# Kernel optimization log

Hardware: AMD Instinct MI355X
Metric: run time of the kernel (lower is better)

## Reference

```python
import jax, jax.numpy as jnp
import numpy as np


def _boxsum(x):
    # x: [C, H, W] -> depthwise 3x3 all-ones sum conv, SAME padding (ChannelWiseSum(C, 3))
    C = x.shape[0]
    k = jnp.ones((C, 1, 3, 3), x.dtype)
    y = jax.lax.conv_general_dilated(
        x[None], k, window_strides=(1, 1), padding='SAME',
        dimension_numbers=('NCHW', 'OIHW', 'NCHW'), feature_group_count=C)
    return y[0]


def setup_inputs() -> dict:
    key = jax.random.key(0)
    k1, k2 = jax.random.split(key)
    H = W = 4096
    rgb = jax.random.uniform(k1, (3, H, W), dtype=jnp.float32)
    # alpha in [0,1] with ~half the pixels exactly 0 so the border diffusion is exercised
    a = jax.random.uniform(k2, (1, H, W), dtype=jnp.float32) * 2.0 - 1.0
    alpha = jnp.maximum(a, 0.0)
    return {"rgb": rgb, "alpha": alpha, "offset": 16}


def reference(rgb, alpha, offset):
    # rgb: [3,H,W], alpha: [1,H,W], offset: python int (number of diffusion steps)
    mask = (alpha > 0.0).astype(rgb.dtype)           # [1,H,W]
    rgb = rgb * mask

    def step(carry, _):
        rgb, mask = carry
        mask_nega = jnp.abs(mask - 1.0)              # [1,H,W], broadcasts over channels
        mask_weight = _boxsum(mask)                  # [1,H,W]
        border = _boxsum(rgb) / (mask_weight + 1e-7) # [3,H,W]
        border = border * mask_nega
        rgb = rgb * mask + border
        mask = (mask_weight > 0.0).astype(rgb.dtype)
        return (rgb, mask), None

    (rgb, _), _ = jax.lax.scan(step, (rgb, mask), None, length=offset)
    return jnp.clip(rgb, 0.0, 1.0)
```

## Files before the change

kernel.cpp:

```cpp
#include <hip/hip_runtime.h>

constexpr int W = 4096;
constexpr int H = 4096;
constexpr int HW = W * H;

constexpr int BX = 32, BY = 8;
constexpr int TILE_W = BX * 4;
constexpr int GRID_X = W / TILE_W;
constexpr int GRID_Y = H / BY;

typedef unsigned char u8;
typedef unsigned int u32;

__device__ __forceinline__ float clamp01(float v) { return fminf(fmaxf(v, 0.f), 1.f); }
__device__ __forceinline__ float4 ld4(const float* p) { return *reinterpret_cast<const float4*>(p); }
__device__ __forceinline__ void st4(float* p, float4 v) { *reinterpret_cast<float4*>(p) = v; }
__device__ __forceinline__ float4 z4() { return make_float4(0.f, 0.f, 0.f, 0.f); }
__device__ __forceinline__ float rcp_f(float x) { return __builtin_amdgcn_rcpf(x); }

__device__ __attribute__((noinline)) u32 far_distance(
    const float* __restrict__ alpha, int x, int y)
{
    for (int dy = -2; dy <= 2; ++dy) {
        int yy = y + dy;
        if (yy < 0 || yy >= H) continue;
        if (dy == -2 || dy == 2) {
            for (int dx = -2; dx <= 2; ++dx) {
                int xx = x + dx;
                if (xx < 0 || xx >= W) continue;
                if (alpha[yy * W + xx] > 0.f) return 2;
            }
        } else {
            if (x - 2 >= 0 && alpha[yy * W + x - 2] > 0.f) return 2;
            if (x + 2 < W && alpha[yy * W + x + 2] > 0.f) return 2;
        }
    }
    for (int r = 3; r <= 16; ++r) {
        bool f = false;
        for (int dx = -r; dx <= r && !f; ++dx) {
            int gx = x + dx;
            if (gx < 0 || gx >= W) continue;
            int gy = y - r;
            if (gy >= 0 && alpha[gy * W + gx] > 0.f) f = true;
            gy = y + r;
            if (!f && gy < H && alpha[gy * W + gx] > 0.f) f = true;
        }
        for (int dy = -r + 1; dy <= r - 1 && !f; ++dy) {
            int gy = y + dy;
            if (gy < 0 || gy >= H) continue;
            int gx = x - r;
            if (gx >= 0 && alpha[gy * W + gx] > 0.f) f = true;
            gx = x + r;
            if (!f && gx < W && alpha[gy * W + gx] > 0.f) f = true;
        }
        if (f) return r;
    }
    return 255;
}

__device__ __forceinline__ float4 plane_vsum(const float* __restrict__ base, int p0,
                                             bool up, bool dn,
                                             float4 mU, float4 mC, float4 mD,
                                             float4* center)
{
    float4 u = up ? ld4(base + p0 - W) : z4();
    float4 c = ld4(base + p0);
    float4 d = dn ? ld4(base + p0 + W) : z4();
    *center = c;
    float4 r;
    r.x = u.x * mU.x + c.x * mC.x + d.x * mD.x;
    r.y = u.y * mU.y + c.y * mC.y + d.y * mD.y;
    r.z = u.z * mU.z + c.z * mC.z + d.z * mD.z;
    r.w = u.w * mU.w + c.w * mC.w + d.w * mD.w;
    return r;
}

__global__ __launch_bounds__(BX * BY) void pass1_kernel(
    const float* __restrict__ rgb, const float* __restrict__ alpha,
    float* __restrict__ out, u8* __restrict__ dmap,
    u32* __restrict__ cnt, int* __restrict__ list, u32 cap)
{
    __shared__ __align__(16) float vs[4][BY][132];

    const int tx = threadIdx.x, ty = threadIdx.y;
    const int x0 = blockIdx.x * TILE_W + tx * 4;
    const int y  = blockIdx.y * BY + ty;
    const int p0 = y * W + x0;

    const bool up = (y > 0), dn = (y < H - 1);

    float4 aU = up ? ld4(alpha + p0 - W) : z4();
    float4 aC = ld4(alpha + p0);
    float4 aD = dn ? ld4(alpha + p0 + W) : z4();

    float4 mU = make_float4(aU.x > 0.f, aU.y > 0.f, aU.z > 0.f, aU.w > 0.f);
    float4 mC = make_float4(aC.x > 0.f, aC.y > 0.f, aC.z > 0.f, aC.w > 0.f);
    float4 mD = make_float4(aD.x > 0.f, aD.y > 0.f, aD.z > 0.f, aD.w > 0.f);

    float4 vwt;
    vwt.x = mU.x + mC.x + mD.x;
    vwt.y = mU.y + mC.y + mD.y;
    vwt.z = mU.z + mC.z + mD.z;
    vwt.w = mU.w + mC.w + mD.w;

    const float* Gp = rgb + HW;
    const float* Bp = rgb + 2 * HW;

    float4 rC, gC, bC;
    float4 vr = plane_vsum(rgb, p0, up, dn, mU, mC, mD, &rC);
    float4 vg = plane_vsum(Gp,  p0, up, dn, mU, mC, mD, &gC);
    float4 vb = plane_vsum(Bp,  p0, up, dn, mU, mC, mD, &bC);

    st4(&vs[0][ty][tx * 4], vr);
    st4(&vs[1][ty][tx * 4], vg);
    st4(&vs[2][ty][tx * 4], vb);
    st4(&vs[3][ty][tx * 4], vwt);

    if (tx == 0 || tx == BX - 1) {
        int xh   = (tx == 0) ? x0 - 1 : x0 + 4;
        int slot = (tx == 0) ? 130 : 128;
        float sr = 0.f, sg = 0.f, sb = 0.f, sw = 0.f;
        if (xh >= 0 && xh < W) {
            #pragma unroll
            for (int dy = -1; dy <= 1; ++dy) {
                int yy = y + dy;
                if (yy < 0 || yy >= H) continue;
                int q = yy * W + xh;
                float m = (alpha[q] > 0.f) ? 1.f : 0.f;
                sw += m;
                sr += m * rgb[q];
                sg += m * Gp[q];
                sb += m * Bp[q];
            }
        }
        vs[0][ty][slot] = sr;
        vs[1][ty][slot] = sg;
        vs[2][ty][slot] = sb;
        vs[3][ty][slot] = sw;
    }
    __syncthreads();

    const int cL = (tx == 0) ? 130 : tx * 4 - 1;
    const int cR = (tx == BX - 1) ? 128 : tx * 4 + 4;

    float sr[4], sg[4], sb[4], sw[4];
    {
        float4 v = ld4(&vs[0][ty][tx * 4]);
        float l = vs[0][ty][cL], r = vs[0][ty][cR];
        sr[0] = l + v.x + v.y; sr[1] = v.x + v.y + v.z;
        sr[2] = v.y + v.z + v.w; sr[3] = v.z + v.w + r;
    }
    {
        float4 v = ld4(&vs[1][ty][tx * 4]);
        float l = vs[1][ty][cL], r = vs[1][ty][cR];
        sg[0] = l + v.x + v.y; sg[1] = v.x + v.y + v.z;
        sg[2] = v.y + v.z + v.w; sg[3] = v.z + v.w + r;
    }
    {
        float4 v = ld4(&vs[2][ty][tx * 4]);
        float l = vs[2][ty][cL], r = vs[2][ty][cR];
        sb[0] = l + v.x + v.y; sb[1] = v.x + v.y + v.z;
        sb[2] = v.y + v.z + v.w; sb[3] = v.z + v.w + r;
    }
    {
        float4 v = ld4(&vs[3][ty][tx * 4]);
        float l = vs[3][ty][cL], r = vs[3][ty][cR];
        sw[0] = l + v.x + v.y; sw[1] = v.x + v.y + v.z;
        sw[2] = v.y + v.z + v.w; sw[3] = v.z + v.w + r;
    }

    const float mca[4] = {mC.x, mC.y, mC.z, mC.w};
    const float rca[4] = {rC.x, rC.y, rC.z, rC.w};
    const float gca[4] = {gC.x, gC.y, gC.z, gC.w};
    const float bca[4] = {bC.x, bC.y, bC.z, bC.w};

    float o_r[4], o_g[4], o_b[4];
    u32 dv[4];

    #pragma unroll
    for (int i = 0; i < 4; ++i) {
        if (mca[i] > 0.f) {
            dv[i] = 0;
            o_r[i] = rca[i]; o_g[i] = gca[i]; o_b[i] = bca[i];
        } else if (sw[i] > 0.f) {
            dv[i] = 1;
            float inv = rcp_f(sw[i] + 1e-7f);
            o_r[i] = sr[i] * inv; o_g[i] = sg[i] * inv; o_b[i] = sb[i] * inv;
        } else {
            u32 d = far_distance(alpha, x0 + i, y);
            dv[i] = d;
            o_r[i] = 0.f; o_g[i] = 0.f; o_b[i] = 0.f;
            if (d >= 3 && d <= 16) {
                u32 idx = atomicAdd(cnt, 1u);
                if (idx < cap) list[idx] = p0 + i;
            }
        }
    }

    st4(out + p0, make_float4(clamp01(o_r[0]), clamp01(o_r[1]),
                              clamp01(o_r[2]), clamp01(o_r[3])));
    st4(out + HW + p0, make_float4(clamp01(o_g[0]), clamp01(o_g[1]),
                                   clamp01(o_g[2]), clamp01(o_g[3])));
    st4(out + 2 * HW + p0, make_float4(clamp01(o_b[0]), clamp01(o_b[1]),
                                       clamp01(o_b[2]), clamp01(o_b[3])));
    *reinterpret_cast<uchar4*>(dmap + p0) =
        make_uchar4((u8)dv[0], (u8)dv[1], (u8)dv[2], (u8)dv[3]);
}

__device__ __forceinline__ void fill_pixel(float* __restrict__ out,
                                           const u8* __restrict__ dmap,
                                           int x, int y, int t)
{
    float s0 = 0.f, s1 = 0.f, s2 = 0.f;
    int cnt = 0;
    #pragma unroll
    for (int dy = -1; dy <= 1; ++dy) {
        int ny = y + dy;
        if (ny < 0 || ny >= H) continue;
        #pragma unroll
        for (int dx = -1; dx <= 1; ++dx) {
            int nx = x + dx;
            if (nx < 0 || nx >= W) continue;
            int q = ny * W + nx;
            if (dmap[q] == (u8)(t - 1)) {
                cnt++;
                s0 += out[q];
                s1 += out[HW + q];
                s2 += out[2 * HW + q];
            }
        }
    }
    float inv = rcp_f((float)cnt + 1e-7f);
    int p = y * W + x;
    out[p]          = clamp01(s0 * inv);
    out[HW + p]     = clamp01(s1 * inv);
    out[2 * HW + p] = clamp01(s2 * inv);
}

__global__ __launch_bounds__(256) void tail_dense(
    float* __restrict__ out, const u8* __restrict__ dmap)
{
    int idx = blockIdx.x * 256 + threadIdx.x;
    int p = idx * 4;
    uchar4 dq = *reinterpret_cast<const uchar4*>(dmap + p);
    if (dq.x != 2 && dq.y != 2 && dq.z != 2 && dq.w != 2) return;
    int y = p >> 12;
    int xb = p & (W - 1);
    if (dq.x == 2) fill_pixel(out, dmap, xb + 0, y, 2);
    if (dq.y == 2) fill_pixel(out, dmap, xb + 1, y, 2);
    if (dq.z == 2) fill_pixel(out, dmap, xb + 2, y, 2);
    if (dq.w == 2) fill_pixel(out, dmap, xb + 3, y, 2);
}

__global__ __launch_bounds__(256) void tail_far(
    float* __restrict__ out, const u8* __restrict__ dmap,
    const int* __restrict__ list, const u32* __restrict__ cnt, u32 cap)
{
    u32 n = *cnt;
    if (n > cap) n = cap;
    for (int t = 3; t <= 16; ++t) {
        for (u32 i = threadIdx.x; i < n; i += 256) {
            int p = list[i];
            if (dmap[p] == (u8)t)
                fill_pixel(out, dmap, p & (W - 1), p >> 12, t);
        }
        __syncthreads();
    }
}

extern "C" void kernel_launch(void* const* d_in, const int* in_sizes, int n_in,
                              void* d_out, int out_size, void* d_ws, size_t ws_size,
                              hipStream_t stream) {
    const float* rgb   = (const float*)d_in[0];
    const float* alpha = (const float*)d_in[1];
    float* out = (float*)d_out;

    u8* dmap  = (u8*)d_ws;
    u32* cnt  = (u32*)((char*)d_ws + HW);
    int* list = (int*)((char*)d_ws + HW + 16);
    u32 cap = 0;
    if (ws_size > (size_t)HW + 16) {
        size_t c = (ws_size - HW - 16) / 4;
        cap = (u32)(c > (1u << 22) ? (1u << 22) : c);
    }

    hipMemsetAsync(cnt, 0, 4, stream);

    pass1_kernel<<<dim3(GRID_X, GRID_Y), dim3(BX, BY), 0, stream>>>(
        rgb, alpha, out, dmap, cnt, list, cap);
    tail_dense<<<HW / 4 / 256, 256, 0, stream>>>(out, dmap);
    tail_far<<<1, 256, 0, stream>>>(out, dmap, list, cnt, cap);
}
```

Before: 170.3 us.

## Replace LDS halo exchange with wavefront shuffles and widen dense tail scan

The block becomes 64x4 so each row maps onto one 64-lane wavefront. The left and right horizontal neighbours of the vertical partial sums now come from __shfl_up/__shfl_down instead of a shared-memory tile, which removes the LDS traffic and the __syncthreads. All nine rgb loads are also issued up front. The dense tail kernel now scans 16 dmap bytes per thread using a SWAR byte-equality test, cutting thread count and load instructions. The risk is that the shuffle path depends on wavefront size 64, and the row edges still need the scalar halo loads.

```diff
diff --git a/kernel.cpp b/kernel.cpp
--- a/kernel.cpp
+++ b/kernel.cpp
@@ -4,7 +4,7 @@
 constexpr int H = 4096;
 constexpr int HW = W * H;
 
-constexpr int BX = 32, BY = 8;
+constexpr int BX = 64, BY = 4;
 constexpr int TILE_W = BX * 4;
 constexpr int GRID_X = W / TILE_W;
 constexpr int GRID_Y = H / BY;
@@ -58,15 +58,9 @@
     return 255;
 }
 
-__device__ __forceinline__ float4 plane_vsum(const float* __restrict__ base, int p0,
-                                             bool up, bool dn,
-                                             float4 mU, float4 mC, float4 mD,
-                                             float4* center)
-{
-    float4 u = up ? ld4(base + p0 - W) : z4();
-    float4 c = ld4(base + p0);
-    float4 d = dn ? ld4(base + p0 + W) : z4();
-    *center = c;
+__device__ __forceinline__ float4 vsum4(float4 u, float4 c, float4 d,
+                                        float4 mU, float4 mC, float4 mD)
+{
     float4 r;
     r.x = u.x * mU.x + c.x * mC.x + d.x * mD.x;
     r.y = u.y * mU.y + c.y * mC.y + d.y * mD.y;
@@ -80,46 +74,50 @@
     float* __restrict__ out, u8* __restrict__ dmap,
     u32* __restrict__ cnt, int* __restrict__ list, u32 cap)
 {
-    __shared__ __align__(16) float vs[4][BY][132];
-
-    const int tx = threadIdx.x, ty = threadIdx.y;
+    const int tx = threadIdx.x;
+    const int ty = threadIdx.y;
     const int x0 = blockIdx.x * TILE_W + tx * 4;
     const int y  = blockIdx.y * BY + ty;
     const int p0 = y * W + x0;
-
     const bool up = (y > 0), dn = (y < H - 1);
+
+    const float* Gp = rgb + HW;
+    const float* Bp = rgb + 2 * HW;
 
     float4 aU = up ? ld4(alpha + p0 - W) : z4();
     float4 aC = ld4(alpha + p0);
     float4 aD = dn ? ld4(alpha + p0 + W) : z4();
+    float4 rU = up ? ld4(rgb + p0 - W) : z4();
+    float4 rC = ld4(rgb + p0);
+    float4 rD = dn ? ld4(rgb + p0 + W) : z4();
+    float4 gU = up ? ld4(Gp + p0 - W) : z4();
+    float4 gC = ld4(Gp + p0);
+    float4 gD = dn ? ld4(Gp + p0 + W) : z4();
+    float4 bU = up ? ld4(Bp + p0 - W) : z4();
+    float4 bC = ld4(Bp + p0);
+    float4 bD = dn ? ld4(Bp + p0 + W) : z4();
 
     float4 mU = make_float4(aU.x > 0.f, aU.y > 0.f, aU.z > 0.f, aU.w > 0.f);
     float4 mC = make_float4(aC.x > 0.f, aC.y > 0.f, aC.z > 0.f, aC.w > 0.f);
     float4 mD = make_float4(aD.x > 0.f, aD.y > 0.f, aD.z > 0.f, aD.w > 0.f);
 
-    float4 vwt;
-    vwt.x = mU.x + mC.x + mD.x;
-    vwt.y = mU.y + mC.y + mD.y;
-    vwt.z = mU.z + mC.z + mD.z;
-    vwt.w = mU.w + mC.w + mD.w;
-
-    const float* Gp = rgb + HW;
-    const float* Bp = rgb + 2 * HW;
-
-    float4 rC, gC, bC;
-    float4 vr = plane_vsum(rgb, p0, up, dn, mU, mC, mD, &rC);
-    float4 vg = plane_vsum(Gp,  p0, up, dn, mU, mC, mD, &gC);
-    float4 vb = plane_vsum(Bp,  p0, up, dn, mU, mC, mD, &bC);
-
-    st4(&vs[0][ty][tx * 4], vr);
-    st4(&vs[1][ty][tx * 4], vg);
-    st4(&vs[2][ty][tx * 4], vb);
-    st4(&vs[3][ty][tx * 4], vwt);
+    float4 vw;
+    vw.x = mU.x + mC.x + mD.x;
+    vw.y = mU.y + mC.y + mD.y;
+    vw.z = mU.z + mC.z + mD.z;
+    vw.w = mU.w + mC.w + mD.w;
+    float4 vr = vsum4(rU, rC, rD, mU, mC, mD);
+    float4 vg = vsum4(gU, gC, gD, mU, mC, mD);
+    float4 vb = vsum4(bU, bC, bD, mU, mC, mD);
+
+    float lw = __shfl_up(vw.w, 1), rw = __shfl_down(vw.x, 1);
+    float lr = __shfl_up(vr.w, 1), rr = __shfl_down(vr.x, 1);
+    float lg = __shfl_up(vg.w, 1), rg = __shfl_down(vg.x, 1);
+    float lb = __shfl_up(vb.w, 1), rb = __shfl_down(vb.x, 1);
 
     if (tx == 0 || tx == BX - 1) {
-        int xh   = (tx == 0) ? x0 - 1 : x0 + 4;
-        int slot = (tx == 0) ? 130 : 128;
-        float sr = 0.f, sg = 0.f, sb = 0.f, sw = 0.f;
+        int xh = (tx == 0) ? x0 - 1 : x0 + 4;
+        float hr = 0.f, hg = 0.f, hb = 0.f, hw = 0.f;
         if (xh >= 0 && xh < W) {
             #pragma unroll
             for (int dy = -1; dy <= 1; ++dy) {
@@ -127,47 +125,24 @@
                 if (yy < 0 || yy >= H) continue;
                 int q = yy * W + xh;
                 float m = (alpha[q] > 0.f) ? 1.f : 0.f;
-                sw += m;
-                sr += m * rgb[q];
-                sg += m * Gp[q];
-                sb += m * Bp[q];
-            }
-        }
-        vs[0][ty][slot] = sr;
-        vs[1][ty][slot] = sg;
-        vs[2][ty][slot] = sb;
-        vs[3][ty][slot] = sw;
-    }
-    __syncthreads();
-
-    const int cL = (tx == 0) ? 130 : tx * 4 - 1;
-    const int cR = (tx == BX - 1) ? 128 : tx * 4 + 4;
-
-    float sr[4], sg[4], sb[4], sw[4];
-    {
-        float4 v = ld4(&vs[0][ty][tx * 4]);
-        float l = vs[0][ty][cL], r = vs[0][ty][cR];
-        sr[0] = l + v.x + v.y; sr[1] = v.x + v.y + v.z;
-        sr[2] = v.y + v.z + v.w; sr[3] = v.z + v.w + r;
-    }
-    {
-        float4 v = ld4(&vs[1][ty][tx * 4]);
-        float l = vs[1][ty][cL], r = vs[1][ty][cR];
-        sg[0] = l + v.x + v.y; sg[1] = v.x + v.y + v.z;
-        sg[2] = v.y + v.z + v.w; sg[3] = v.z + v.w + r;
-    }
-    {
-        float4 v = ld4(&vs[2][ty][tx * 4]);
-        float l = vs[2][ty][cL], r = vs[2][ty][cR];
-        sb[0] = l + v.x + v.y; sb[1] = v.x + v.y + v.z;
-        sb[2] = v.y + v.z + v.w; sb[3] = v.z + v.w + r;
-    }
-    {
-        float4 v = ld4(&vs[3][ty][tx * 4]);
-        float l = vs[3][ty][cL], r = vs[3][ty][cR];
-        sw[0] = l + v.x + v.y; sw[1] = v.x + v.y + v.z;
-        sw[2] = v.y + v.z + v.w; sw[3] = v.z + v.w + r;
-    }
+                hw += m;
+                hr += m * rgb[q];
+                hg += m * Gp[q];
+                hb += m * Bp[q];
+            }
+        }
+        if (tx == 0) { lw = hw; lr = hr; lg = hg; lb = hb; }
+        else         { rw = hw; rr = hr; rg = hg; rb = hb; }
+    }
+
+    float sw[4] = { lw + vw.x + vw.y, vw.x + vw.y + vw.z,
+                    vw.y + vw.z + vw.w, vw.z + vw.w + rw };
+    float sr[4] = { lr + vr.x + vr.y, vr.x + vr.y + vr.z,
+                    vr.y + vr.z + vr.w, vr.z + vr.w + rr };
+    float sg[4] = { lg + vg.x + vg.y, vg.x + vg.y + vg.z,
+                    vg.y + vg.z + vg.w, vg.z + vg.w + rg };
+    float sb[4] = { lb + vb.x + vb.y, vb.x + vb.y + vb.z,
+                    vb.y + vb.z + vb.w, vb.z + vb.w + rb };
 
     const float mca[4] = {mC.x, mC.y, mC.z, mC.w};
     const float rca[4] = {rC.x, rC.y, rC.z, rC.w};
@@ -237,19 +212,31 @@
     out[2 * HW + p] = clamp01(s2 * inv);
 }
 
+__device__ __forceinline__ u32 has_byte2(u32 x) {
+    u32 v = x ^ 0x02020202u;
+    return (v - 0x01010101u) & ~v & 0x80808080u;
+}
+
 __global__ __launch_bounds__(256) void tail_dense(
     float* __restrict__ out, const u8* __restrict__ dmap)
 {
     int idx = blockIdx.x * 256 + threadIdx.x;
-    int p = idx * 4;
-    uchar4 dq = *reinterpret_cast<const uchar4*>(dmap + p);
-    if (dq.x != 2 && dq.y != 2 && dq.z != 2 && dq.w != 2) return;
+    int p = idx * 16;
+    uint4 dq = *reinterpret_cast<const uint4*>(dmap + p);
+    if (!(has_byte2(dq.x) | has_byte2(dq.y) | has_byte2(dq.z) | has_byte2(dq.w)))
+        return;
     int y = p >> 12;
     int xb = p & (W - 1);
-    if (dq.x == 2) fill_pixel(out, dmap, xb + 0, y, 2);
-    if (dq.y == 2) fill_pixel(out, dmap, xb + 1, y, 2);
-    if (dq.z == 2) fill_pixel(out, dmap, xb + 2, y, 2);
-    if (dq.w == 2) fill_pixel(out, dmap, xb + 3, y, 2);
+    u32 words[4] = {dq.x, dq.y, dq.z, dq.w};
+    #pragma unroll
+    for (int wi = 0; wi < 4; ++wi) {
+        u32 v = words[wi];
+        #pragma unroll
+        for (int b = 0; b < 4; ++b) {
+            if (((v >> (8 * b)) & 0xFFu) == 2u)
+                fill_pixel(out, dmap, xb + wi * 4 + b, y, 2);
+        }
+    }
 }
 
 __global__ __launch_bounds__(256) void tail_far(
@@ -288,6 +275,6 @@
 
     pass1_kernel<<<dim3(GRID_X, GRID_Y), dim3(BX, BY), 0, stream>>>(
         rgb, alpha, out, dmap, cnt, list, cap);
-    tail_dense<<<HW / 4 / 256, 256, 0, stream>>>(out, dmap);
+    tail_dense<<<HW / 16 / 256, 256, 0, stream>>>(out, dmap);
     tail_far<<<1, 256, 0, stream>>>(out, dmap, list, cnt, cap);
 }
```

New measurement: 158.3 us. 1.08x faster.
